# Performance work log

Measured on AMD Instinct MI355X. Metric: run time of the kernel, lower is better.

Reference implementation:

```python
import jax, jax.numpy as jnp
import numpy as np

V, D, K = 50000, 300, 50      # vocab, embed_dim, dim_latent (topics)
B, S, N, L = 32, 8192, 128, 64  # batch, doc len, segments/doc, max seg len (=stride)


def setup_inputs() -> dict:
    key = jax.random.key(0)
    k0, k1, k2, k3, k4, k5 = jax.random.split(key, 6)
    embedding = jax.random.normal(k0, (V, D), jnp.float32) * 0.02
    M_w = jax.random.normal(k1, (D, D), jnp.float32) / np.sqrt(D).astype(np.float32)
    W_w = jax.random.normal(k2, (K, D), jnp.float32) / np.sqrt(D).astype(np.float32)
    T_w = jax.random.normal(k3, (D, K), jnp.float32) / np.sqrt(K).astype(np.float32)
    input_tensor = jax.random.randint(k4, (B, S), 0, V)
    # non-overlapping segments with stride L; ragged lengths in [8, L]
    seg_starts = jnp.broadcast_to(jnp.arange(N, dtype=jnp.int32) * L, (B, N))
    seg_lens = jax.random.randint(k5, (B, N), 8, L + 1)
    return {"embedding": embedding, "M_w": M_w, "W_w": W_w, "T_w": T_w,
            "input_tensor": input_tensor, "seg_starts": seg_starts, "seg_lens": seg_lens}


def reference(embedding, M_w, W_w, T_w, input_tensor, seg_starts, seg_lens):
    # Build padded segment token grid + mask (vectorized version of the
    # per-batch Python loop in the original forward).
    offs = jnp.arange(L)
    pos = seg_starts[..., None] + offs                       # [B,N,L]
    mask = (offs < seg_lens[..., None]).astype(embedding.dtype)  # [B,N,L]
    tok = jnp.take_along_axis(input_tensor, pos.reshape(B, N * L), axis=1).reshape(B, N, L)
    sub_emb = embedding[tok] * mask[..., None]               # [B,N,L,D] (zeros at pad)
    # masked mean over segment tokens
    y = sub_emb.sum(axis=2) / jnp.maximum(mask.sum(axis=2), 1.0)[..., None]  # [B,N,D]
    # attention score: (M @ e_l) . y, masked softmax
    esc = jnp.einsum('bnld,ed,bne->bnl', sub_emb, M_w, y)    # M(x) = x @ M_w.T
    esc = jnp.where(mask > 0, esc, -1e9)
    alpha = jax.nn.softmax(esc, axis=-1)                     # [B,N,L]
    z = jnp.einsum('bnl,bnld->bnd', alpha, sub_emb)          # [B,N,D]
    p = jax.nn.softmax(z @ W_w.T, axis=-1)                   # [B,N,K]
    r = p @ T_w.T                                            # [B,N,D]
    return y, z, p, r
```

## Files before the change

kernel.cpp:

```cpp
#include <hip/hip_runtime.h>

#define DD 300
#define KK 50
#define BB 32
#define SS 8192
#define NN 128
#define LL 64
#define NSEG (BB * NN)
#define NW 5
#define NT 320
#define NJ 13
#define NC 5
#define TM 8

__device__ __forceinline__ float wave_sum(float v) {
    #pragma unroll
    for (int m = 32; m; m >>= 1) v += __shfl_xor(v, m, 64);
    return v;
}
__device__ __forceinline__ float wave_max(float v) {
    #pragma unroll
    for (int m = 32; m; m >>= 1) v = fmaxf(v, __shfl_xor(v, m, 64));
    return v;
}

__global__ __launch_bounds__(NT) void k_y(
    const float* __restrict__ emb,
    const int*   __restrict__ tokens,
    const int*   __restrict__ seg_starts,
    const int*   __restrict__ seg_lens,
    float* __restrict__ out_y)
{
    __shared__ int   tok_s[LL];
    __shared__ float part[NW][NT];

    const int tid  = threadIdx.x;
    const int wave = tid >> 6;
    const int lane = tid & 63;
    const int seg  = blockIdx.x;
    const int b    = seg >> 7;
    const int start = seg_starts[seg];
    const int len   = seg_lens[seg];

    if (tid < LL) tok_s[tid] = tokens[b * SS + start + tid];
    __syncthreads();

    float rr[NJ][NC];
    #pragma unroll
    for (int j = 0; j < NJ; ++j) {
        const int l  = wave + j * NW;
        const int lc = (l < len) ? l : (len - 1);
        const float* row = emb + (size_t)tok_s[lc] * DD;
        rr[j][0] = row[lane];
        rr[j][1] = row[lane + 64];
        rr[j][2] = row[lane + 128];
        rr[j][3] = row[lane + 192];
        rr[j][4] = (lane < 44) ? row[lane + 256] : 0.f;
    }
    float acc[NC] = {0.f, 0.f, 0.f, 0.f, 0.f};
    #pragma unroll
    for (int j = 0; j < NJ; ++j) {
        const int l = wave + j * NW;
        const float m = (l < len) ? 1.f : 0.f;
        #pragma unroll
        for (int c = 0; c < NC; ++c) acc[c] += m * rr[j][c];
    }
    #pragma unroll
    for (int c = 0; c < NC; ++c) part[wave][lane + 64 * c] = acc[c];
    __syncthreads();

    if (tid < DD) {
        const float s = part[0][tid] + part[1][tid] + part[2][tid] + part[3][tid] + part[4][tid];
        out_y[(size_t)seg * DD + tid] = s / (float)len;
    }
}

__global__ __launch_bounds__(NT) void k_u(
    const float* __restrict__ y,
    const float* __restrict__ M_w,
    float* __restrict__ u)
{
    const int tid  = threadIdx.x;
    const int row0 = blockIdx.x * TM;
    if (tid >= DD) return;

    float acc[TM];
    #pragma unroll
    for (int r = 0; r < TM; ++r) acc[r] = 0.f;

    #pragma unroll 5
    for (int e = 0; e < DD; ++e) {
        const float m = M_w[(size_t)e * DD + tid];
        #pragma unroll
        for (int r = 0; r < TM; ++r)
            acc[r] += m * y[(size_t)(row0 + r) * DD + e];
    }
    #pragma unroll
    for (int r = 0; r < TM; ++r)
        u[(size_t)(row0 + r) * DD + tid] = acc[r];
}

__global__ __launch_bounds__(NT) void k_rest(
    const float* __restrict__ emb,
    const float* __restrict__ W_w,
    const float* __restrict__ T_w,
    const int*   __restrict__ tokens,
    const int*   __restrict__ seg_starts,
    const int*   __restrict__ seg_lens,
    const float* __restrict__ u_ws,
    float* __restrict__ out_z,
    float* __restrict__ out_p,
    float* __restrict__ out_r)
{
    __shared__ int   tok_s[LL];
    __shared__ float a_s[LL + 1];
    __shared__ float zp_s[NW][NT];
    __shared__ float z_s[NT];
    __shared__ float p_s[64];

    const int tid  = threadIdx.x;
    const int wave = tid >> 6;
    const int lane = tid & 63;
    const int seg  = blockIdx.x;
    const int b    = seg >> 7;
    const int start = seg_starts[seg];
    const int len   = seg_lens[seg];

    if (tid < LL) tok_s[tid] = tokens[b * SS + start + tid];
    __syncthreads();

    float uu[NC];
    {
        const float* up = u_ws + (size_t)seg * DD;
        uu[0] = up[lane];
        uu[1] = up[lane + 64];
        uu[2] = up[lane + 128];
        uu[3] = up[lane + 192];
        uu[4] = (lane < 44) ? up[lane + 256] : 0.f;
    }

    float rr[NJ][NC];
    #pragma unroll
    for (int j = 0; j < NJ; ++j) {
        const int l  = wave + j * NW;
        const int lc = (l < len) ? l : (len - 1);
        const float* row = emb + (size_t)tok_s[lc] * DD;
        rr[j][0] = row[lane];
        rr[j][1] = row[lane + 64];
        rr[j][2] = row[lane + 128];
        rr[j][3] = row[lane + 192];
        rr[j][4] = (lane < 44) ? row[lane + 256] : 0.f;
    }

    #pragma unroll
    for (int j = 0; j < NJ; ++j) {
        const int l = wave + j * NW;
        float dot = rr[j][0] * uu[0] + rr[j][1] * uu[1] + rr[j][2] * uu[2]
                  + rr[j][3] * uu[3] + rr[j][4] * uu[4];
        dot = wave_sum(dot);
        if (lane == 0 && l < len) a_s[l] = dot;
    }
    __syncthreads();

    if (wave == 0) {
        const float v  = (lane < len) ? a_s[lane] : -INFINITY;
        const float mx = wave_max(v);
        const float e  = (lane < len) ? __expf(v - mx) : 0.f;
        const float sm = wave_sum(e);
        a_s[lane] = e / sm;
    }
    if (tid == NT - 1) a_s[LL] = 0.f;
    __syncthreads();

    {
        float zacc[NC] = {0.f, 0.f, 0.f, 0.f, 0.f};
        #pragma unroll
        for (int j = 0; j < NJ; ++j) {
            const int l = wave + j * NW;
            const float a = a_s[l];
            #pragma unroll
            for (int c = 0; c < NC; ++c) zacc[c] += a * rr[j][c];
        }
        #pragma unroll
        for (int c = 0; c < NC; ++c) zp_s[wave][lane + 64 * c] = zacc[c];
    }
    __syncthreads();

    if (tid < DD) {
        const float zv = zp_s[0][tid] + zp_s[1][tid] + zp_s[2][tid] + zp_s[3][tid] + zp_s[4][tid];
        z_s[tid] = zv;
        out_z[(size_t)seg * DD + tid] = zv;
    }
    __syncthreads();

    for (int k = wave; k < KK; k += NW) {
        const float* wr = W_w + (size_t)k * DD;
        float d0 = wr[lane] * z_s[lane] + wr[lane + 64] * z_s[lane + 64]
                 + wr[lane + 128] * z_s[lane + 128] + wr[lane + 192] * z_s[lane + 192];
        if (lane < 44) d0 += wr[lane + 256] * z_s[lane + 256];
        d0 = wave_sum(d0);
        if (lane == 0) p_s[k] = d0;
    }
    __syncthreads();

    if (wave == 0) {
        const float v  = (lane < KK) ? p_s[lane] : -INFINITY;
        const float mx = wave_max(v);
        const float e  = (lane < KK) ? __expf(v - mx) : 0.f;
        const float sm = wave_sum(e);
        if (lane < KK) {
            const float p = e / sm;
            p_s[lane] = p;
            out_p[(size_t)seg * KK + lane] = p;
        }
    }
    __syncthreads();

    if (tid < DD) {
        const float* trow = T_w + (size_t)tid * KK;
        float acc = 0.f;
        #pragma unroll
        for (int k = 0; k < KK; ++k) acc += p_s[k] * trow[k];
        out_r[(size_t)seg * DD + tid] = acc;
    }
}

extern "C" void kernel_launch(void* const* d_in, const int* in_sizes, int n_in,
                              void* d_out, int out_size, void* d_ws, size_t ws_size,
                              hipStream_t stream) {
    const float* emb        = (const float*)d_in[0];
    const float* M_w        = (const float*)d_in[1];
    const float* W_w        = (const float*)d_in[2];
    const float* T_w        = (const float*)d_in[3];
    const int*   tokens     = (const int*)d_in[4];
    const int*   seg_starts = (const int*)d_in[5];
    const int*   seg_lens   = (const int*)d_in[6];

    float* out   = (float*)d_out;
    float* out_y = out;
    float* out_z = out + (size_t)NSEG * DD;
    float* out_p = out + (size_t)2 * NSEG * DD;
    float* out_r = out + (size_t)2 * NSEG * DD + (size_t)NSEG * KK;

    float* u_ws = (float*)d_ws;

    hipLaunchKernelGGL(k_y, dim3(NSEG), dim3(NT), 0, stream,
                       emb, tokens, seg_starts, seg_lens, out_y);
    hipLaunchKernelGGL(k_u, dim3(NSEG / TM), dim3(NT), 0, stream,
                       out_y, M_w, u_ws);
    hipLaunchKernelGGL(k_rest, dim3(NSEG), dim3(NT), 0, stream,
                       emb, W_w, T_w, tokens, seg_starts, seg_lens,
                       u_ws, out_z, out_p, out_r);
}
```

Baseline: 182.1 us.

## Vectorize embedding loads and stage rows in fp16 shared memory

Embedding rows are now read with float4 loads in both the y and rest kernels, and the per-thread register tile of gathered rows is removed. In the rest kernel, rows are packed to half precision into a shared-memory buffer and re-read from there for the weighted sum that produces z. The aim is to cut register pressure and raise occupancy while issuing fewer, wider memory transactions. In exchange, z is accumulated from fp16-rounded embeddings, which can cost accuracy, and the larger shared-memory footprint (about 38KB) may itself limit how many blocks fit per CU.

```diff
diff --git a/kernel.cpp b/kernel.cpp
--- a/kernel.cpp
+++ b/kernel.cpp
@@ -1,4 +1,5 @@
 #include <hip/hip_runtime.h>
+#include <hip/hip_fp16.h>
 
 #define DD 300
 #define KK 50
@@ -10,7 +11,6 @@
 #define NW 5
 #define NT 320
 #define NJ 13
-#define NC 5
 #define TM 8
 
 __device__ __forceinline__ float wave_sum(float v) {
@@ -22,6 +22,14 @@
     #pragma unroll
     for (int m = 32; m; m >>= 1) v = fmaxf(v, __shfl_xor(v, m, 64));
     return v;
+}
+__device__ __forceinline__ unsigned int pack_h2(float a, float b) {
+    __half2 h = __floats2half2_rn(a, b);
+    return *reinterpret_cast<const unsigned int*>(&h);
+}
+__device__ __forceinline__ float2 unpack_h2(unsigned int v) {
+    __half2 h = *reinterpret_cast<const __half2*>(&v);
+    return __half22float2(h);
 }
 
 __global__ __launch_bounds__(NT) void k_y(
@@ -31,8 +39,8 @@
     const int*   __restrict__ seg_lens,
     float* __restrict__ out_y)
 {
-    __shared__ int   tok_s[LL];
-    __shared__ float part[NW][NT];
+    __shared__ int    tok_s[LL];
+    __shared__ float4 part4[NW][75];
 
     const int tid  = threadIdx.x;
     const int wave = tid >> 6;
@@ -45,33 +53,34 @@
     if (tid < LL) tok_s[tid] = tokens[b * SS + start + tid];
     __syncthreads();
 
-    float rr[NJ][NC];
+    float4 a0 = {0.f, 0.f, 0.f, 0.f};
+    float4 a1 = {0.f, 0.f, 0.f, 0.f};
     #pragma unroll
     for (int j = 0; j < NJ; ++j) {
         const int l  = wave + j * NW;
         const int lc = (l < len) ? l : (len - 1);
-        const float* row = emb + (size_t)tok_s[lc] * DD;
-        rr[j][0] = row[lane];
-        rr[j][1] = row[lane + 64];
-        rr[j][2] = row[lane + 128];
-        rr[j][3] = row[lane + 192];
-        rr[j][4] = (lane < 44) ? row[lane + 256] : 0.f;
-    }
-    float acc[NC] = {0.f, 0.f, 0.f, 0.f, 0.f};
-    #pragma unroll
-    for (int j = 0; j < NJ; ++j) {
-        const int l = wave + j * NW;
+        const float4* row4 = (const float4*)(emb + (size_t)tok_s[lc] * DD);
+        const float4 r0 = row4[lane];
+        float4 r1 = {0.f, 0.f, 0.f, 0.f};
+        if (lane < 11) r1 = row4[64 + lane];
         const float m = (l < len) ? 1.f : 0.f;
-        #pragma unroll
-        for (int c = 0; c < NC; ++c) acc[c] += m * rr[j][c];
-    }
-    #pragma unroll
-    for (int c = 0; c < NC; ++c) part[wave][lane + 64 * c] = acc[c];
-    __syncthreads();
-
-    if (tid < DD) {
-        const float s = part[0][tid] + part[1][tid] + part[2][tid] + part[3][tid] + part[4][tid];
-        out_y[(size_t)seg * DD + tid] = s / (float)len;
+        a0.x += m * r0.x; a0.y += m * r0.y; a0.z += m * r0.z; a0.w += m * r0.w;
+        a1.x += m * r1.x; a1.y += m * r1.y; a1.z += m * r1.z; a1.w += m * r1.w;
+    }
+    part4[wave][lane] = a0;
+    if (lane < 11) part4[wave][64 + lane] = a1;
+    __syncthreads();
+
+    if (tid < 75) {
+        float4 s = {0.f, 0.f, 0.f, 0.f};
+        #pragma unroll
+        for (int w = 0; w < NW; ++w) {
+            const float4 pv = part4[w][tid];
+            s.x += pv.x; s.y += pv.y; s.z += pv.z; s.w += pv.w;
+        }
+        const float inv = 1.f / (float)len;
+        s.x *= inv; s.y *= inv; s.z *= inv; s.w *= inv;
+        ((float4*)(out_y + (size_t)seg * DD))[tid] = s;
     }
 }
 
@@ -112,11 +121,12 @@
     float* __restrict__ out_p,
     float* __restrict__ out_r)
 {
-    __shared__ int   tok_s[LL];
-    __shared__ float a_s[LL + 1];
-    __shared__ float zp_s[NW][NT];
-    __shared__ float z_s[NT];
-    __shared__ float p_s[64];
+    __shared__ int    tok_s[LL];
+    __shared__ uint2  e_s[LL][75];
+    __shared__ float  a_s[LL + 1];
+    __shared__ float2 zp_s[NW][150];
+    __shared__ float  z_s[NT];
+    __shared__ float  p_s[64];
 
     const int tid  = threadIdx.x;
     const int wave = tid >> 6;
@@ -129,37 +139,34 @@
     if (tid < LL) tok_s[tid] = tokens[b * SS + start + tid];
     __syncthreads();
 
-    float uu[NC];
+    float4 u0, u1 = {0.f, 0.f, 0.f, 0.f};
     {
-        const float* up = u_ws + (size_t)seg * DD;
-        uu[0] = up[lane];
-        uu[1] = up[lane + 64];
-        uu[2] = up[lane + 128];
-        uu[3] = up[lane + 192];
-        uu[4] = (lane < 44) ? up[lane + 256] : 0.f;
-    }
-
-    float rr[NJ][NC];
+        const float4* up4 = (const float4*)(u_ws + (size_t)seg * DD);
+        u0 = up4[lane];
+        if (lane < 11) u1 = up4[64 + lane];
+    }
+
     #pragma unroll
     for (int j = 0; j < NJ; ++j) {
         const int l  = wave + j * NW;
         const int lc = (l < len) ? l : (len - 1);
-        const float* row = emb + (size_t)tok_s[lc] * DD;
-        rr[j][0] = row[lane];
-        rr[j][1] = row[lane + 64];
-        rr[j][2] = row[lane + 128];
-        rr[j][3] = row[lane + 192];
-        rr[j][4] = (lane < 44) ? row[lane + 256] : 0.f;
-    }
-
-    #pragma unroll
-    for (int j = 0; j < NJ; ++j) {
-        const int l = wave + j * NW;
-        float dot = rr[j][0] * uu[0] + rr[j][1] * uu[1] + rr[j][2] * uu[2]
-                  + rr[j][3] * uu[3] + rr[j][4] * uu[4];
+        const float4* row4 = (const float4*)(emb + (size_t)tok_s[lc] * DD);
+        const float4 r0 = row4[lane];
+        float4 r1 = {0.f, 0.f, 0.f, 0.f};
+        if (lane < 11) r1 = row4[64 + lane];
+
+        if (l < LL) {
+            e_s[l][lane] = make_uint2(pack_h2(r0.x, r0.y), pack_h2(r0.z, r0.w));
+            if (lane < 11)
+                e_s[l][64 + lane] = make_uint2(pack_h2(r1.x, r1.y), pack_h2(r1.z, r1.w));
+        }
+
+        float dot = r0.x * u0.x + r0.y * u0.y + r0.z * u0.z + r0.w * u0.w
+                  + r1.x * u1.x + r1.y * u1.y + r1.z * u1.z + r1.w * u1.w;
         dot = wave_sum(dot);
         if (lane == 0 && l < len) a_s[l] = dot;
     }
+    if (tid == NT - 1) a_s[LL] = 0.f;
     __syncthreads();
 
     if (wave == 0) {
@@ -169,27 +176,41 @@
         const float sm = wave_sum(e);
         a_s[lane] = e / sm;
     }
-    if (tid == NT - 1) a_s[LL] = 0.f;
     __syncthreads();
 
     {
-        float zacc[NC] = {0.f, 0.f, 0.f, 0.f, 0.f};
+        float2 zA = {0.f, 0.f}, zB = {0.f, 0.f}, zC = {0.f, 0.f};
         #pragma unroll
         for (int j = 0; j < NJ; ++j) {
-            const int l = wave + j * NW;
+            const int l  = wave + j * NW;
+            const int lr = (l < LL) ? l : (LL - 1);
             const float a = a_s[l];
-            #pragma unroll
-            for (int c = 0; c < NC; ++c) zacc[c] += a * rr[j][c];
-        }
-        #pragma unroll
-        for (int c = 0; c < NC; ++c) zp_s[wave][lane + 64 * c] = zacc[c];
-    }
-    __syncthreads();
-
-    if (tid < DD) {
-        const float zv = zp_s[0][tid] + zp_s[1][tid] + zp_s[2][tid] + zp_s[3][tid] + zp_s[4][tid];
-        z_s[tid] = zv;
-        out_z[(size_t)seg * DD + tid] = zv;
+            const unsigned int* ru = (const unsigned int*)&e_s[lr][0];
+            const float2 fA = unpack_h2(ru[lane]);
+            const float2 fB = unpack_h2(ru[64 + lane]);
+            zA.x += a * fA.x; zA.y += a * fA.y;
+            zB.x += a * fB.x; zB.y += a * fB.y;
+            if (lane < 22) {
+                const float2 fC = unpack_h2(ru[128 + lane]);
+                zC.x += a * fC.x; zC.y += a * fC.y;
+            }
+        }
+        zp_s[wave][lane]      = zA;
+        zp_s[wave][64 + lane] = zB;
+        if (lane < 22) zp_s[wave][128 + lane] = zC;
+    }
+    __syncthreads();
+
+    if (tid < 150) {
+        float2 s = {0.f, 0.f};
+        #pragma unroll
+        for (int w = 0; w < NW; ++w) {
+            const float2 pv = zp_s[w][tid];
+            s.x += pv.x; s.y += pv.y;
+        }
+        z_s[2 * tid]     = s.x;
+        z_s[2 * tid + 1] = s.y;
+        ((float2*)(out_z + (size_t)seg * DD))[tid] = s;
     }
     __syncthreads();
 
```

After: 224.4 us. +23.2%, slower.

## Gather fp16 copy of embedding table with one wave per segment

Applied to the files above, without the earlier changes.

Converts the embedding table and the W/T weights to padded fp16 in workspace each call. The y and attention kernels are rewritten so that one wave processes one segment, using 16-byte half loads, double-buffered gathers and shuffle-based reductions instead of shared memory. The aim is to halve the bytes moved by the random row gathers, at the cost of a full-table conversion pass per call and reduced precision. A fallback keeps the fp32 path when the workspace is too small.

```diff
diff --git a/kernel.cpp b/kernel.cpp
--- a/kernel.cpp
+++ b/kernel.cpp
@@ -1,4 +1,5 @@
 #include <hip/hip_runtime.h>
+#include <hip/hip_fp16.h>
 
 #define DD 300
 #define KK 50
@@ -7,11 +8,18 @@
 #define NN 128
 #define LL 64
 #define NSEG (BB * NN)
+#define HH 304
+#define TMU 8
+#define NTU 320
 #define NW 5
 #define NT 320
 #define NJ 13
 #define NC 5
-#define TM 8
+
+#define EMB16_BYTES ((size_t)50000 * HH * 2)
+#define U_BYTES     ((size_t)NSEG * DD * 4)
+#define W16_BYTES   ((size_t)KK * HH * 2)
+#define T16_BYTES   ((size_t)64 * HH * 2)
 
 __device__ __forceinline__ float wave_sum(float v) {
     #pragma unroll
@@ -24,198 +32,378 @@
     return v;
 }
 
-__global__ __launch_bounds__(NT) void k_y(
-    const float* __restrict__ emb,
-    const int*   __restrict__ tokens,
-    const int*   __restrict__ seg_starts,
-    const int*   __restrict__ seg_lens,
+__device__ __forceinline__ float dot8(uint4 r, const float u8[8]) {
+    const float2 f0 = __half22float2(*(const __half2*)&r.x);
+    const float2 f1 = __half22float2(*(const __half2*)&r.y);
+    const float2 f2 = __half22float2(*(const __half2*)&r.z);
+    const float2 f3 = __half22float2(*(const __half2*)&r.w);
+    return f0.x*u8[0] + f0.y*u8[1] + f1.x*u8[2] + f1.y*u8[3]
+         + f2.x*u8[4] + f2.y*u8[5] + f3.x*u8[6] + f3.y*u8[7];
+}
+__device__ __forceinline__ void fma8(float z8[8], float a, uint4 r) {
+    const float2 f0 = __half22float2(*(const __half2*)&r.x);
+    const float2 f1 = __half22float2(*(const __half2*)&r.y);
+    const float2 f2 = __half22float2(*(const __half2*)&r.z);
+    const float2 f3 = __half22float2(*(const __half2*)&r.w);
+    z8[0] += a*f0.x; z8[1] += a*f0.y; z8[2] += a*f1.x; z8[3] += a*f1.y;
+    z8[4] += a*f2.x; z8[5] += a*f2.y; z8[6] += a*f3.x; z8[7] += a*f3.y;
+}
+__device__ __forceinline__ void ld4e(const __half* __restrict__ E, int tok, int len,
+                                     int l0, int c, uint4* R) {
+    #pragma unroll
+    for (int i = 0; i < 4; ++i) {
+        int lc = l0 + i; lc = (lc < len) ? lc : (len - 1);
+        const int t = __shfl(tok, lc);
+        if (c < 38) R[i] = *(const uint4*)(E + (size_t)t * HH + 8 * c);
+    }
+}
+__device__ __forceinline__ void ld4h(const __half* __restrict__ M, int rmax,
+                                     int r0, int c, uint4* R) {
+    #pragma unroll
+    for (int i = 0; i < 4; ++i) {
+        int rc = r0 + i; rc = (rc < rmax) ? rc : rmax;
+        if (c < 38) R[i] = *(const uint4*)(M + (size_t)rc * HH + 8 * c);
+    }
+}
+__device__ __forceinline__ void store300(float* out, int c, const float z8[8]) {
+    float4* o4 = (float4*)out;
+    if (c < 37) {
+        o4[2*c]   = make_float4(z8[0], z8[1], z8[2], z8[3]);
+        o4[2*c+1] = make_float4(z8[4], z8[5], z8[6], z8[7]);
+    } else if (c == 37) {
+        o4[74]    = make_float4(z8[0], z8[1], z8[2], z8[3]);
+    }
+}
+
+__global__ __launch_bounds__(256) void k_cvt_emb(const float* __restrict__ emb,
+                                                 __half* __restrict__ emb16) {
+    const int id = blockIdx.x * 256 + threadIdx.x;
+    if (id >= 50000 * 76) return;
+    const int row = id / 76;
+    const int c4  = (id - row * 76) * 4;
+    float4 v = make_float4(0.f, 0.f, 0.f, 0.f);
+    if (c4 < DD) v = *(const float4*)(emb + (size_t)row * DD + c4);
+    const __half2 h0 = __floats2half2_rn(v.x, v.y);
+    const __half2 h1 = __floats2half2_rn(v.z, v.w);
+    uint2 pk;
+    pk.x = *(const unsigned int*)&h0;
+    pk.y = *(const unsigned int*)&h1;
+    *(uint2*)(emb16 + (size_t)row * HH + c4) = pk;
+}
+__global__ __launch_bounds__(256) void k_cvt_small(const float* __restrict__ W_w,
+                                                   const float* __restrict__ T_w,
+                                                   __half* __restrict__ W16,
+                                                   __half* __restrict__ T16) {
+    int id = blockIdx.x * 256 + threadIdx.x;
+    if (id < KK * HH) {
+        const int k = id / HH, d = id - k * HH;
+        W16[id] = __float2half((d < DD) ? W_w[(size_t)k * DD + d] : 0.f);
+        return;
+    }
+    id -= KK * HH;
+    if (id < 64 * HH) {
+        const int k = id / HH, d = id - k * HH;
+        T16[id] = __float2half((k < KK && d < DD) ? T_w[(size_t)d * KK + k] : 0.f);
+    }
+}
+
+__global__ __launch_bounds__(256, 4) void k_y16(
+    const __half* __restrict__ emb16,
+    const int* __restrict__ tokens,
+    const int* __restrict__ seg_starts,
+    const int* __restrict__ seg_lens,
     float* __restrict__ out_y)
 {
-    __shared__ int   tok_s[LL];
-    __shared__ float part[NW][NT];
-
-    const int tid  = threadIdx.x;
-    const int wave = tid >> 6;
-    const int lane = tid & 63;
-    const int seg  = blockIdx.x;
-    const int b    = seg >> 7;
-    const int start = seg_starts[seg];
-    const int len   = seg_lens[seg];
-
-    if (tid < LL) tok_s[tid] = tokens[b * SS + start + tid];
-    __syncthreads();
-
-    float rr[NJ][NC];
-    #pragma unroll
-    for (int j = 0; j < NJ; ++j) {
-        const int l  = wave + j * NW;
-        const int lc = (l < len) ? l : (len - 1);
-        const float* row = emb + (size_t)tok_s[lc] * DD;
-        rr[j][0] = row[lane];
-        rr[j][1] = row[lane + 64];
-        rr[j][2] = row[lane + 128];
-        rr[j][3] = row[lane + 192];
-        rr[j][4] = (lane < 44) ? row[lane + 256] : 0.f;
-    }
-    float acc[NC] = {0.f, 0.f, 0.f, 0.f, 0.f};
-    #pragma unroll
-    for (int j = 0; j < NJ; ++j) {
-        const int l = wave + j * NW;
-        const float m = (l < len) ? 1.f : 0.f;
-        #pragma unroll
-        for (int c = 0; c < NC; ++c) acc[c] += m * rr[j][c];
-    }
-    #pragma unroll
-    for (int c = 0; c < NC; ++c) part[wave][lane + 64 * c] = acc[c];
-    __syncthreads();
-
-    if (tid < DD) {
-        const float s = part[0][tid] + part[1][tid] + part[2][tid] + part[3][tid] + part[4][tid];
-        out_y[(size_t)seg * DD + tid] = s / (float)len;
-    }
-}
-
-__global__ __launch_bounds__(NT) void k_u(
+    const int lane = threadIdx.x & 63;
+    const int seg  = blockIdx.x * 4 + (threadIdx.x >> 6);
+    const int len  = seg_lens[seg];
+    const int base = (seg >> 7) * SS + seg_starts[seg];
+    const int tok  = tokens[base + lane];
+    const int c    = lane;
+
+    uint4 A0[4] = {}, A1[4] = {};
+    float a8[8] = {0.f,0.f,0.f,0.f,0.f,0.f,0.f,0.f};
+
+    const int len8 = (len + 7) & ~7;
+    ld4e(emb16, tok, len, 0, c, A0);
+    for (int l0 = 0; l0 < len8; l0 += 8) {
+        ld4e(emb16, tok, len, l0 + 4, c, A1);
+        #pragma unroll
+        for (int i = 0; i < 4; ++i) {
+            const float m = (l0 + i < len) ? 1.f : 0.f;
+            fma8(a8, m, A0[i]);
+        }
+        ld4e(emb16, tok, len, l0 + 8, c, A0);
+        #pragma unroll
+        for (int i = 0; i < 4; ++i) {
+            const float m = (l0 + 4 + i < len) ? 1.f : 0.f;
+            fma8(a8, m, A1[i]);
+        }
+    }
+    const float inv = 1.f / (float)len;
+    #pragma unroll
+    for (int i = 0; i < 8; ++i) a8[i] *= inv;
+    store300(out_y + (size_t)seg * DD, c, a8);
+}
+
+__global__ __launch_bounds__(NTU) void k_u(
     const float* __restrict__ y,
     const float* __restrict__ M_w,
     float* __restrict__ u)
 {
     const int tid  = threadIdx.x;
-    const int row0 = blockIdx.x * TM;
+    const int row0 = blockIdx.x * TMU;
     if (tid >= DD) return;
 
-    float acc[TM];
-    #pragma unroll
-    for (int r = 0; r < TM; ++r) acc[r] = 0.f;
+    float acc[TMU];
+    #pragma unroll
+    for (int r = 0; r < TMU; ++r) acc[r] = 0.f;
 
     #pragma unroll 5
     for (int e = 0; e < DD; ++e) {
         const float m = M_w[(size_t)e * DD + tid];
         #pragma unroll
-        for (int r = 0; r < TM; ++r)
+        for (int r = 0; r < TMU; ++r)
             acc[r] += m * y[(size_t)(row0 + r) * DD + e];
     }
     #pragma unroll
-    for (int r = 0; r < TM; ++r)
+    for (int r = 0; r < TMU; ++r)
         u[(size_t)(row0 + r) * DD + tid] = acc[r];
 }
 
-__global__ __launch_bounds__(NT) void k_rest(
-    const float* __restrict__ emb,
-    const float* __restrict__ W_w,
-    const float* __restrict__ T_w,
-    const int*   __restrict__ tokens,
-    const int*   __restrict__ seg_starts,
-    const int*   __restrict__ seg_lens,
+__global__ __launch_bounds__(256, 4) void k_rest16(
+    const __half* __restrict__ emb16,
+    const __half* __restrict__ W16,
+    const __half* __restrict__ T16,
+    const int* __restrict__ tokens,
+    const int* __restrict__ seg_starts,
+    const int* __restrict__ seg_lens,
     const float* __restrict__ u_ws,
     float* __restrict__ out_z,
     float* __restrict__ out_p,
     float* __restrict__ out_r)
+{
+    const int lane = threadIdx.x & 63;
+    const int seg  = blockIdx.x * 4 + (threadIdx.x >> 6);
+    const int len  = seg_lens[seg];
+    const int base = (seg >> 7) * SS + seg_starts[seg];
+    const int tok  = tokens[base + lane];
+    const int c    = lane;
+
+    float u8[8] = {0.f,0.f,0.f,0.f,0.f,0.f,0.f,0.f};
+    {
+        const float4* u4 = (const float4*)(u_ws + (size_t)seg * DD);
+        if (c < 38) {
+            const float4 a = u4[2*c];
+            u8[0]=a.x; u8[1]=a.y; u8[2]=a.z; u8[3]=a.w;
+            if (c < 37) { const float4 b = u4[2*c+1]; u8[4]=b.x; u8[5]=b.y; u8[6]=b.z; u8[7]=b.w; }
+        }
+    }
+
+    uint4 A0[4] = {}, A1[4] = {};
+
+    float esc = 0.f;
+    const int len8 = (len + 7) & ~7;
+    ld4e(emb16, tok, len, 0, c, A0);
+    for (int l0 = 0; l0 < len8; l0 += 8) {
+        ld4e(emb16, tok, len, l0 + 4, c, A1);
+        {
+            float d0 = dot8(A0[0], u8), d1 = dot8(A0[1], u8);
+            float d2 = dot8(A0[2], u8), d3 = dot8(A0[3], u8);
+            d0 = wave_sum(d0); d1 = wave_sum(d1); d2 = wave_sum(d2); d3 = wave_sum(d3);
+            esc = (lane == l0+0) ? d0 : esc; esc = (lane == l0+1) ? d1 : esc;
+            esc = (lane == l0+2) ? d2 : esc; esc = (lane == l0+3) ? d3 : esc;
+        }
+        ld4e(emb16, tok, len, l0 + 8, c, A0);
+        {
+            float d0 = dot8(A1[0], u8), d1 = dot8(A1[1], u8);
+            float d2 = dot8(A1[2], u8), d3 = dot8(A1[3], u8);
+            d0 = wave_sum(d0); d1 = wave_sum(d1); d2 = wave_sum(d2); d3 = wave_sum(d3);
+            esc = (lane == l0+4) ? d0 : esc; esc = (lane == l0+5) ? d1 : esc;
+            esc = (lane == l0+6) ? d2 : esc; esc = (lane == l0+7) ? d3 : esc;
+        }
+    }
+
+    const float v  = (lane < len) ? esc : -INFINITY;
+    const float mx = wave_max(v);
+    const float ex = (lane < len) ? __expf(v - mx) : 0.f;
+    const float sm = wave_sum(ex);
+    const float alpha = ex / sm;
+
+    float z8[8] = {0.f,0.f,0.f,0.f,0.f,0.f,0.f,0.f};
+    ld4e(emb16, tok, len, 0, c, A0);
+    for (int l0 = 0; l0 < len8; l0 += 8) {
+        ld4e(emb16, tok, len, l0 + 4, c, A1);
+        #pragma unroll
+        for (int i = 0; i < 4; ++i) { const float a = __shfl(alpha, l0 + i);     fma8(z8, a, A0[i]); }
+        ld4e(emb16, tok, len, l0 + 8, c, A0);
+        #pragma unroll
+        for (int i = 0; i < 4; ++i) { const float a = __shfl(alpha, l0 + 4 + i); fma8(z8, a, A1[i]); }
+    }
+    store300(out_z + (size_t)seg * DD, c, z8);
+
+    float sc = 0.f;
+    ld4h(W16, KK - 1, 0, c, A0);
+    for (int k0 = 0; k0 < 56; k0 += 8) {
+        ld4h(W16, KK - 1, k0 + 4, c, A1);
+        {
+            float t0 = dot8(A0[0], z8), t1 = dot8(A0[1], z8);
+            float t2 = dot8(A0[2], z8), t3 = dot8(A0[3], z8);
+            t0 = wave_sum(t0); t1 = wave_sum(t1); t2 = wave_sum(t2); t3 = wave_sum(t3);
+            sc = (lane == k0+0) ? t0 : sc; sc = (lane == k0+1) ? t1 : sc;
+            sc = (lane == k0+2) ? t2 : sc; sc = (lane == k0+3) ? t3 : sc;
+        }
+        ld4h(W16, KK - 1, k0 + 8, c, A0);
+        {
+            float t0 = dot8(A1[0], z8), t1 = dot8(A1[1], z8);
+            float t2 = dot8(A1[2], z8), t3 = dot8(A1[3], z8);
+            t0 = wave_sum(t0); t1 = wave_sum(t1); t2 = wave_sum(t2); t3 = wave_sum(t3);
+            sc = (lane == k0+4) ? t0 : sc; sc = (lane == k0+5) ? t1 : sc;
+            sc = (lane == k0+6) ? t2 : sc; sc = (lane == k0+7) ? t3 : sc;
+        }
+    }
+    const float vk  = (lane < KK) ? sc : -INFINITY;
+    const float mxk = wave_max(vk);
+    const float ek  = (lane < KK) ? __expf(vk - mxk) : 0.f;
+    const float smk = wave_sum(ek);
+    const float p   = ek / smk;
+    if (lane < KK) out_p[(size_t)seg * KK + lane] = p;
+
+    float r8[8] = {0.f,0.f,0.f,0.f,0.f,0.f,0.f,0.f};
+    ld4h(T16, 63, 0, c, A0);
+    for (int k0 = 0; k0 < 56; k0 += 8) {
+        ld4h(T16, 63, k0 + 4, c, A1);
+        #pragma unroll
+        for (int i = 0; i < 4; ++i) { const float pk = __shfl(p, k0 + i);     fma8(r8, pk, A0[i]); }
+        ld4h(T16, 63, k0 + 8, c, A0);
+        #pragma unroll
+        for (int i = 0; i < 4; ++i) { const float pk = __shfl(p, k0 + 4 + i); fma8(r8, pk, A1[i]); }
+    }
+    store300(out_r + (size_t)seg * DD, c, r8);
+}
+
+__global__ __launch_bounds__(NT) void fb_y(
+    const float* __restrict__ emb, const int* __restrict__ tokens,
+    const int* __restrict__ seg_starts, const int* __restrict__ seg_lens,
+    float* __restrict__ out_y)
+{
+    __shared__ int   tok_s[LL];
+    __shared__ float part[NW][NT];
+    const int tid = threadIdx.x, wave = tid >> 6, lane = tid & 63;
+    const int seg = blockIdx.x, b = seg >> 7;
+    const int start = seg_starts[seg], len = seg_lens[seg];
+    if (tid < LL) tok_s[tid] = tokens[b * SS + start + tid];
+    __syncthreads();
+    float rr[NJ][NC];
+    #pragma unroll
+    for (int j = 0; j < NJ; ++j) {
+        const int l = wave + j * NW;
+        const int lc = (l < len) ? l : (len - 1);
+        const float* row = emb + (size_t)tok_s[lc] * DD;
+        rr[j][0] = row[lane]; rr[j][1] = row[lane+64]; rr[j][2] = row[lane+128];
+        rr[j][3] = row[lane+192]; rr[j][4] = (lane < 44) ? row[lane+256] : 0.f;
+    }
+    float acc[NC] = {0.f,0.f,0.f,0.f,0.f};
+    #pragma unroll
+    for (int j = 0; j < NJ; ++j) {
+        const int l = wave + j * NW;
+        const float m = (l < len) ? 1.f : 0.f;
+        #pragma unroll
+        for (int cc = 0; cc < NC; ++cc) acc[cc] += m * rr[j][cc];
+    }
+    #pragma unroll
+    for (int cc = 0; cc < NC; ++cc) part[wave][lane + 64*cc] = acc[cc];
+    __syncthreads();
+    if (tid < DD) {
+        const float s = part[0][tid]+part[1][tid]+part[2][tid]+part[3][tid]+part[4][tid];
+        out_y[(size_t)seg * DD + tid] = s / (float)len;
+    }
+}
+__global__ __launch_bounds__(NT) void fb_rest(
+    const float* __restrict__ emb, const float* __restrict__ W_w,
+    const float* __restrict__ T_w, const int* __restrict__ tokens,
+    const int* __restrict__ seg_starts, const int* __restrict__ seg_lens,
+    const float* __restrict__ u_ws, float* __restrict__ out_z,
+    float* __restrict__ out_p, float* __restrict__ out_r)
 {
     __shared__ int   tok_s[LL];
     __shared__ float a_s[LL + 1];
     __shared__ float zp_s[NW][NT];
     __shared__ float z_s[NT];
     __shared__ float p_s[64];
-
-    const int tid  = threadIdx.x;
-    const int wave = tid >> 6;
-    const int lane = tid & 63;
-    const int seg  = blockIdx.x;
-    const int b    = seg >> 7;
-    const int start = seg_starts[seg];
-    const int len   = seg_lens[seg];
-
+    const int tid = threadIdx.x, wave = tid >> 6, lane = tid & 63;
+    const int seg = blockIdx.x, b = seg >> 7;
+    const int start = seg_starts[seg], len = seg_lens[seg];
     if (tid < LL) tok_s[tid] = tokens[b * SS + start + tid];
     __syncthreads();
-
     float uu[NC];
     {
         const float* up = u_ws + (size_t)seg * DD;
-        uu[0] = up[lane];
-        uu[1] = up[lane + 64];
-        uu[2] = up[lane + 128];
-        uu[3] = up[lane + 192];
-        uu[4] = (lane < 44) ? up[lane + 256] : 0.f;
-    }
-
+        uu[0]=up[lane]; uu[1]=up[lane+64]; uu[2]=up[lane+128]; uu[3]=up[lane+192];
+        uu[4]=(lane < 44) ? up[lane+256] : 0.f;
+    }
     float rr[NJ][NC];
     #pragma unroll
     for (int j = 0; j < NJ; ++j) {
-        const int l  = wave + j * NW;
+        const int l = wave + j * NW;
         const int lc = (l < len) ? l : (len - 1);
         const float* row = emb + (size_t)tok_s[lc] * DD;
-        rr[j][0] = row[lane];
-        rr[j][1] = row[lane + 64];
-        rr[j][2] = row[lane + 128];
-        rr[j][3] = row[lane + 192];
-        rr[j][4] = (lane < 44) ? row[lane + 256] : 0.f;
-    }
-
+        rr[j][0]=row[lane]; rr[j][1]=row[lane+64]; rr[j][2]=row[lane+128];
+        rr[j][3]=row[lane+192]; rr[j][4]=(lane<44)?row[lane+256]:0.f;
+    }
     #pragma unroll
     for (int j = 0; j < NJ; ++j) {
         const int l = wave + j * NW;
-        float dot = rr[j][0] * uu[0] + rr[j][1] * uu[1] + rr[j][2] * uu[2]
-                  + rr[j][3] * uu[3] + rr[j][4] * uu[4];
+        float dot = rr[j][0]*uu[0]+rr[j][1]*uu[1]+rr[j][2]*uu[2]+rr[j][3]*uu[3]+rr[j][4]*uu[4];
         dot = wave_sum(dot);
         if (lane == 0 && l < len) a_s[l] = dot;
     }
     __syncthreads();
-
     if (wave == 0) {
-        const float v  = (lane < len) ? a_s[lane] : -INFINITY;
-        const float mx = wave_max(v);
-        const float e  = (lane < len) ? __expf(v - mx) : 0.f;
+        const float vv = (lane < len) ? a_s[lane] : -INFINITY;
+        const float mx = wave_max(vv);
+        const float e  = (lane < len) ? __expf(vv - mx) : 0.f;
         const float sm = wave_sum(e);
         a_s[lane] = e / sm;
     }
     if (tid == NT - 1) a_s[LL] = 0.f;
     __syncthreads();
-
     {
-        float zacc[NC] = {0.f, 0.f, 0.f, 0.f, 0.f};
+        float zacc[NC] = {0.f,0.f,0.f,0.f,0.f};
         #pragma unroll
         for (int j = 0; j < NJ; ++j) {
             const int l = wave + j * NW;
             const float a = a_s[l];
             #pragma unroll
-            for (int c = 0; c < NC; ++c) zacc[c] += a * rr[j][c];
-        }
-        #pragma unroll
-        for (int c = 0; c < NC; ++c) zp_s[wave][lane + 64 * c] = zacc[c];
-    }
-    __syncthreads();
-
+            for (int cc = 0; cc < NC; ++cc) zacc[cc] += a * rr[j][cc];
+        }
+        #pragma unroll
+        for (int cc = 0; cc < NC; ++cc) zp_s[wave][lane + 64*cc] = zacc[cc];
+    }
+    __syncthreads();
     if (tid < DD) {
-        const float zv = zp_s[0][tid] + zp_s[1][tid] + zp_s[2][tid] + zp_s[3][tid] + zp_s[4][tid];
+        const float zv = zp_s[0][tid]+zp_s[1][tid]+zp_s[2][tid]+zp_s[3][tid]+zp_s[4][tid];
         z_s[tid] = zv;
         out_z[(size_t)seg * DD + tid] = zv;
     }
     __syncthreads();
-
     for (int k = wave; k < KK; k += NW) {
         const float* wr = W_w + (size_t)k * DD;
-        float d0 = wr[lane] * z_s[lane] + wr[lane + 64] * z_s[lane + 64]
-                 + wr[lane + 128] * z_s[lane + 128] + wr[lane + 192] * z_s[lane + 192];
-        if (lane < 44) d0 += wr[lane + 256] * z_s[lane + 256];
+        float d0 = wr[lane]*z_s[lane] + wr[lane+64]*z_s[lane+64]
+                 + wr[lane+128]*z_s[lane+128] + wr[lane+192]*z_s[lane+192];
+        if (lane < 44) d0 += wr[lane+256]*z_s[lane+256];
         d0 = wave_sum(d0);
         if (lane == 0) p_s[k] = d0;
     }
     __syncthreads();
-
     if (wave == 0) {
-        const float v  = (lane < KK) ? p_s[lane] : -INFINITY;
-        const float mx = wave_max(v);
-        const float e  = (lane < KK) ? __expf(v - mx) : 0.f;
+        const float vv = (lane < KK) ? p_s[lane] : -INFINITY;
+        const float mx = wave_max(vv);
+        const float e  = (lane < KK) ? __expf(vv - mx) : 0.f;
         const float sm = wave_sum(e);
-        if (lane < KK) {
-            const float p = e / sm;
-            p_s[lane] = p;
-            out_p[(size_t)seg * KK + lane] = p;
-        }
-    }
-    __syncthreads();
-
+        if (lane < KK) { const float p = e/sm; p_s[lane] = p; out_p[(size_t)seg*KK+lane] = p; }
+    }
+    __syncthreads();
     if (tid < DD) {
         const float* trow = T_w + (size_t)tid * KK;
         float acc = 0.f;
@@ -242,13 +430,34 @@
     float* out_p = out + (size_t)2 * NSEG * DD;
     float* out_r = out + (size_t)2 * NSEG * DD + (size_t)NSEG * KK;
 
-    float* u_ws = (float*)d_ws;
-
-    hipLaunchKernelGGL(k_y, dim3(NSEG), dim3(NT), 0, stream,
-                       emb, tokens, seg_starts, seg_lens, out_y);
-    hipLaunchKernelGGL(k_u, dim3(NSEG / TM), dim3(NT), 0, stream,
-                       out_y, M_w, u_ws);
-    hipLaunchKernelGGL(k_rest, dim3(NSEG), dim3(NT), 0, stream,
-                       emb, W_w, T_w, tokens, seg_starts, seg_lens,
-                       u_ws, out_z, out_p, out_r);
-}
+    char* ws = (char*)d_ws;
+    const size_t need = EMB16_BYTES + U_BYTES + W16_BYTES + T16_BYTES;
+
+    if (ws_size >= need) {
+        __half* emb16 = (__half*)ws;
+        float*  u_ws  = (float*)(ws + EMB16_BYTES);
+        __half* W16   = (__half*)(ws + EMB16_BYTES + U_BYTES);
+        __half* T16   = (__half*)(ws + EMB16_BYTES + U_BYTES + W16_BYTES);
+
+        hipLaunchKernelGGL(k_cvt_emb, dim3((50000*76 + 255)/256), dim3(256), 0, stream,
+                           emb, emb16);
+        hipLaunchKernelGGL(k_cvt_small, dim3(((KK+64)*HH + 255)/256), dim3(256), 0, stream,
+                           W_w, T_w, W16, T16);
+        hipLaunchKernelGGL(k_y16, dim3(NSEG/4), dim3(256), 0, stream,
+                           emb16, tokens, seg_starts, seg_lens, out_y);
+        hipLaunchKernelGGL(k_u, dim3(NSEG/TMU), dim3(NTU), 0, stream,
+                           out_y, M_w, u_ws);
+        hipLaunchKernelGGL(k_rest16, dim3(NSEG/4), dim3(256), 0, stream,
+                           emb16, W16, T16, tokens, seg_starts, seg_lens,
+                           u_ws, out_z, out_p, out_r);
+    } else {
+        float* u_ws = (float*)ws;
+        hipLaunchKernelGGL(fb_y, dim3(NSEG), dim3(NT), 0, stream,
+                           emb, tokens, seg_starts, seg_lens, out_y);
+        hipLaunchKernelGGL(k_u, dim3(NSEG/TMU), dim3(NTU), 0, stream,
+                           out_y, M_w, u_ws);
+        hipLaunchKernelGGL(fb_rest, dim3(NSEG), dim3(NT), 0, stream,
+                           emb, W_w, T_w, tokens, seg_starts, seg_lens,
+                           u_ws, out_z, out_p, out_r);
+    }
+}
```

After: 292.5 us. +60.6%, slower.
